# Kernel optimization log

Measured on AMD Instinct MI355X. Metric: run time of the kernel, lower is better.

## Reference

```python
import jax, jax.numpy as jnp
import numpy as np

D_MODEL = 1024
N_HEADS = 16
D_HEAD = D_MODEL // N_HEADS  # 64
D_VALUE = 64
D_FFN = 4096
B, T = 2, 2048
LN_EPS = 1e-5


def setup_inputs() -> dict:
    key = jax.random.key(0)
    ks = jax.random.split(key, 8)
    s = 0.02
    return {
        "x": jax.random.normal(ks[0], (B, T, D_MODEL), jnp.float32),
        "ln1_w": jnp.ones((D_MODEL,), jnp.float32),
        "ln1_b": jnp.zeros((D_MODEL,), jnp.float32),
        "Wq": jax.random.normal(ks[1], (D_MODEL, N_HEADS * D_HEAD), jnp.float32) * s,
        "Wk": jax.random.normal(ks[2], (D_MODEL, N_HEADS * D_HEAD), jnp.float32) * s,
        "Wv": jax.random.normal(ks[3], (D_MODEL, N_HEADS * D_VALUE), jnp.float32) * s,
        "Wo": jax.random.normal(ks[4], (N_HEADS * D_VALUE, D_MODEL), jnp.float32) * s,
        "ln2_w": jnp.ones((D_MODEL,), jnp.float32),
        "ln2_b": jnp.zeros((D_MODEL,), jnp.float32),
        "W1": jax.random.normal(ks[5], (D_MODEL, D_FFN), jnp.float32) * s,
        "W2": jax.random.normal(ks[6], (D_FFN, D_MODEL), jnp.float32) * s,
    }


def _layernorm(x, w, b):
    mu = jnp.mean(x, axis=-1, keepdims=True)
    var = jnp.mean(jnp.square(x - mu), axis=-1, keepdims=True)
    return (x - mu) * jax.lax.rsqrt(var + LN_EPS) * w + b


def reference(x, ln1_w, ln1_b, Wq, Wk, Wv, Wo, ln2_w, ln2_b, W1, W2):
    Bd, Td, Dd = x.shape
    h = _layernorm(x, ln1_w, ln1_b)
    # project and split heads: [B, H, T, d]
    Q = (h @ Wq).reshape(Bd, Td, N_HEADS, D_HEAD).transpose(0, 2, 1, 3)
    K = (h @ Wk).reshape(Bd, Td, N_HEADS, D_HEAD).transpose(0, 2, 1, 3)
    V = (h @ Wv).reshape(Bd, Td, N_HEADS, D_VALUE).transpose(0, 2, 1, 3)
    scale = 1.0 / np.sqrt(D_HEAD).astype(np.float32)
    scores = jnp.einsum("bhqd,bhkd->bhqk", Q, K) * scale  # [B,H,T,T]
    causal = jnp.tril(jnp.ones((Td, Td), bool))
    scores = jnp.where(causal[None, None], scores, -jnp.inf)
    attn = jax.nn.softmax(scores, axis=-1)
    out = jnp.einsum("bhqk,bhkd->bhqd", attn, V)  # [B,H,T,dv]
    out = out.transpose(0, 2, 1, 3).reshape(Bd, Td, N_HEADS * D_VALUE)
    x = x + out @ Wo
    h2 = _layernorm(x, ln2_w, ln2_b)
    # torch nn.GELU default is exact erf
    ffn = jax.nn.gelu(h2 @ W1, approximate=False) @ W2
    return x + ffn
```

## Files before the change

### kernel.cpp

```cpp
#include <hip/hip_runtime.h>

using short4_t = __attribute__((ext_vector_type(4))) short;
using short8_t = __attribute__((ext_vector_type(8))) short;
using f32x4    = __attribute__((ext_vector_type(4))) float;

#define B_SZ 2
#define T_SZ 2048
#define DM   1024
#define MROWS (B_SZ * T_SZ)

#define BAR() asm volatile("s_barrier" ::: "memory")

__device__ __forceinline__ unsigned short f2bf(float f) {
  unsigned u = __builtin_bit_cast(unsigned, f);
  return (unsigned short)((u + 0x7FFFu + ((u >> 16) & 1u)) >> 16);
}
__device__ __forceinline__ float bf2f(unsigned short u) {
  return __builtin_bit_cast(float, (unsigned)u << 16);
}

__device__ __forceinline__ f32x4 mfma32(short8_t a, short8_t b, f32x4 c) {
  return __builtin_amdgcn_mfma_f32_16x16x32_bf16(a, b, c, 0, 0, 0);
}
__device__ __forceinline__ f32x4 mfma16(short4_t a, short4_t b, f32x4 c) {
  return __builtin_amdgcn_mfma_f32_16x16x16bf16_1k(a, b, c, 0, 0, 0);
}

__device__ __forceinline__ void gload16(const void* g, void* l) {
  __builtin_amdgcn_global_load_lds(
      (const __attribute__((address_space(1))) unsigned int*)g,
      (__attribute__((address_space(3))) unsigned int*)l, 16, 0, 0);
}

__global__ __launch_bounds__(256) void transpose_all(
    const float* __restrict__ Wq, const float* __restrict__ Wk,
    const float* __restrict__ Wv, const float* __restrict__ Wo,
    const float* __restrict__ W1, const float* __restrict__ W2,
    unsigned short* __restrict__ WqkvT, unsigned short* __restrict__ WoT,
    unsigned short* __restrict__ W1T, unsigned short* __restrict__ W2T) {
  const int bid = blockIdx.x;
  const float* in;
  unsigned short* outp;
  int K, N, tn, tk;
  if (bid < 4096) {
    const int m = bid >> 10, t = bid & 1023;
    K = 1024; N = 1024; tn = t & 31; tk = t >> 5;
    in = (m == 0) ? Wq : (m == 1) ? Wk : (m == 2) ? Wv : Wo;
    outp = (m == 3) ? WoT : (WqkvT + (size_t)m * 1024 * 1024);
  } else if (bid < 8192) {
    const int t = bid - 4096;
    K = 1024; N = 4096; tn = t & 127; tk = t >> 7;
    in = W1; outp = W1T;
  } else {
    const int t = bid - 8192;
    K = 4096; N = 1024; tn = t & 31; tk = t >> 5;
    in = W2; outp = W2T;
  }
  __shared__ float tile[32][33];
  const int tx = threadIdx.x & 31, ty = threadIdx.x >> 5;
  const int n0 = tn * 32, k0 = tk * 32;
#pragma unroll
  for (int i = 0; i < 4; ++i)
    tile[ty + 8 * i][tx] = in[(size_t)(k0 + ty + 8 * i) * N + n0 + tx];
  __syncthreads();
#pragma unroll
  for (int i = 0; i < 4; ++i)
    outp[(size_t)(n0 + ty + 8 * i) * K + k0 + tx] = f2bf(tile[tx][ty + 8 * i]);
}

__global__ __launch_bounds__(256) void ln_kernel(
    const float* __restrict__ X, const float* __restrict__ W,
    const float* __restrict__ Bb, unsigned short* __restrict__ Out) {
  const int row = blockIdx.x, tid = threadIdx.x;
  const float4 v = *(const float4*)(X + (size_t)row * DM + tid * 4);
  float s1 = v.x + v.y + v.z + v.w;
  float s2 = v.x * v.x + v.y * v.y + v.z * v.z + v.w * v.w;
#pragma unroll
  for (int m = 1; m < 64; m <<= 1) {
    s1 += __shfl_xor(s1, m);
    s2 += __shfl_xor(s2, m);
  }
  __shared__ float red[8];
  const int wave = tid >> 6, lane = tid & 63;
  if (lane == 0) { red[wave * 2] = s1; red[wave * 2 + 1] = s2; }
  __syncthreads();
  const float S1 = red[0] + red[2] + red[4] + red[6];
  const float S2 = red[1] + red[3] + red[5] + red[7];
  const float mu = S1 * (1.0f / DM);
  const float var = S2 * (1.0f / DM) - mu * mu;
  const float rs = rsqrtf(var + 1e-5f);
  const float4 w = *(const float4*)(W + tid * 4);
  const float4 b = *(const float4*)(Bb + tid * 4);
  ushort4 o;
  o.x = f2bf((v.x - mu) * rs * w.x + b.x);
  o.y = f2bf((v.y - mu) * rs * w.y + b.y);
  o.z = f2bf((v.z - mu) * rs * w.z + b.z);
  o.w = f2bf((v.w - mu) * rs * w.w + b.w);
  *(ushort4*)(Out + (size_t)row * DM + tid * 4) = o;
}

template <int EPI>
__global__ __launch_bounds__(512, 2) void gemm8(
    const unsigned short* __restrict__ A, const unsigned short* __restrict__ Bt,
    const float* __restrict__ Res, void* __restrict__ Out,
    unsigned short* __restrict__ P01, unsigned short* __restrict__ P23,
    int N, int K, int Ksplit) {
  __shared__ char lds[3][32768];
  const int tid = threadIdx.x;
  const int lane = tid & 63;
  const int wave = tid >> 6;
  const int lr = lane & 15, lg = lane >> 4;
  const int wm = wave >> 2, wn = wave & 3;
  const int row0 = blockIdx.y * 256, col0 = blockIdx.x * 256;
  const int k0 = blockIdx.z * Ksplit;
  const int NT = Ksplit >> 5;

  size_t aoff[2], boff[2];
#pragma unroll
  for (int j = 0; j < 2; ++j) {
    const int o = j * 8192 + tid * 16;
    const int lrow = o >> 7, w = o & 127;
    const int u = w ^ ((lrow & 7) << 4);
    const int grow = lrow + ((u >> 6) << 7);
    const int gk = (u & 63) >> 1;
    aoff[j] = (size_t)(row0 + grow) * K + k0 + gk;
    boff[j] = (size_t)(col0 + grow) * K + k0 + gk;
  }
  const int axor = ((wm << 6) | (lg << 4)) ^ ((lr & 7) << 4);
  const int bxor = (((wn >> 1) << 6) | (lg << 4)) ^ ((lr & 7) << 4);
  const int arow = lr * 128;
  const int brow = ((wn & 1) * 64 + lr) * 128;

  f32x4 acc[8][4] = {};

#pragma unroll
  for (int t = 0; t < 2; ++t) {
#pragma unroll
    for (int j = 0; j < 2; ++j)
      gload16(A + aoff[j] + t * 32, &lds[t][0] + j * 8192 + tid * 16);
#pragma unroll
    for (int j = 0; j < 2; ++j)
      gload16(Bt + boff[j] + t * 32, &lds[t][0] + 16384 + j * 8192 + tid * 16);
  }
  asm volatile("s_waitcnt vmcnt(4)" ::: "memory");
  BAR();

  int bc = 0;
  for (int t = 0; t < NT; ++t) {
    const char* Acur = &lds[bc][0];
    const char* Bcur = Acur + 16384;
    int sb = bc + 2; if (sb >= 3) sb -= 3;
    char* Stg = &lds[sb][0];
    const int tko = (t + 2 < NT) ? (t + 2) * 32 : (NT - 1) * 32;

    short8_t af[4], bf[4];
#pragma unroll
    for (int rs = 0; rs < 4; ++rs)
      af[rs] = *(const short8_t*)(Acur + arow + rs * 2048 + axor);
#pragma unroll
    for (int cs = 0; cs < 4; ++cs)
      bf[cs] = *(const short8_t*)(Bcur + brow + cs * 2048 + bxor);
#pragma unroll
    for (int j = 0; j < 2; ++j)
      gload16(A + aoff[j] + tko, Stg + j * 8192 + tid * 16);
    BAR();
    __builtin_amdgcn_s_setprio(1);
#pragma unroll
    for (int rs = 0; rs < 4; ++rs)
#pragma unroll
      for (int cs = 0; cs < 4; ++cs)
        acc[rs][cs] = mfma32(af[rs], bf[cs], acc[rs][cs]);
    __builtin_amdgcn_s_setprio(0);
    BAR();

#pragma unroll
    for (int rs = 0; rs < 4; ++rs)
      af[rs] = *(const short8_t*)(Acur + arow + (rs + 4) * 2048 + axor);
#pragma unroll
    for (int j = 0; j < 2; ++j)
      gload16(Bt + boff[j] + tko, Stg + 16384 + j * 8192 + tid * 16);
    BAR();
    __builtin_amdgcn_s_setprio(1);
#pragma unroll
    for (int rs = 0; rs < 4; ++rs)
#pragma unroll
      for (int cs = 0; cs < 4; ++cs)
        acc[rs + 4][cs] = mfma32(af[rs], bf[cs], acc[rs + 4][cs]);
    __builtin_amdgcn_s_setprio(0);
    asm volatile("s_waitcnt vmcnt(4)" ::: "memory");
    BAR();
    bc = (bc == 2) ? 0 : bc + 1;
  }
  asm volatile("s_waitcnt vmcnt(0)" ::: "memory");

#pragma unroll
  for (int rs = 0; rs < 8; ++rs)
#pragma unroll
    for (int cs = 0; cs < 4; ++cs) {
      const int gr = row0 + wm * 128 + rs * 16 + lg * 4;
      const int gc = col0 + wn * 64 + cs * 16 + lr;
#pragma unroll
      for (int r = 0; r < 4; ++r) {
        const float v = acc[rs][cs][r];
        const size_t idx = (size_t)(gr + r) * N + gc;
        if (EPI == 0) {
          ((unsigned short*)Out)[idx] = f2bf(v);
        } else if (EPI == 1) {
          ((float*)Out)[idx] = v + Res[idx];
        } else if (EPI == 2) {
          const float g = 0.5f * v * (1.0f + erff(v * 0.70710678118654752f));
          ((unsigned short*)Out)[idx] = f2bf(g);
        } else {
          unsigned short* P = (blockIdx.z >> 1) ? P23 : P01;
          P[(size_t)(blockIdx.z & 1) * MROWS * 1024 + idx] = f2bf(v);
        }
      }
    }
}

__global__ __launch_bounds__(256) void reduce_ffn2(
    const float* __restrict__ X2,
    const unsigned short* __restrict__ P0, const unsigned short* __restrict__ P1,
    const unsigned short* __restrict__ P2, const unsigned short* __restrict__ P3,
    int ns, float* __restrict__ Out) {
  const size_t i = ((size_t)blockIdx.x * 256 + threadIdx.x) * 4;
  float4 o = *(const float4*)(X2 + i);
  ushort4 a = *(const ushort4*)(P0 + i);
  ushort4 b = *(const ushort4*)(P1 + i);
  o.x += bf2f(a.x) + bf2f(b.x);
  o.y += bf2f(a.y) + bf2f(b.y);
  o.z += bf2f(a.z) + bf2f(b.z);
  o.w += bf2f(a.w) + bf2f(b.w);
  if (ns == 4) {
    ushort4 c = *(const ushort4*)(P2 + i);
    ushort4 d = *(const ushort4*)(P3 + i);
    o.x += bf2f(c.x) + bf2f(d.x);
    o.y += bf2f(c.y) + bf2f(d.y);
    o.z += bf2f(c.z) + bf2f(d.z);
    o.w += bf2f(c.w) + bf2f(d.w);
  }
  *(float4*)(Out + i) = o;
}

__device__ __forceinline__ void attn_tile(
    const unsigned short* Kcur, const unsigned short* Vcur,
    const short8_t* qf, f32x4* acc, float& l_run, bool diag) {
  const int tid = threadIdx.x;
  const int lane = tid & 63, wave = tid >> 6;
  const int lr = lane & 15, lg = lane >> 4;
  const float C2 = 0.18033688011112042f;
  float pv[4][4];
  float psum = 0.f;
#pragma unroll
  for (int st = 0; st < 4; ++st) {
    f32x4 s = {0.f, 0.f, 0.f, 0.f};
#pragma unroll
    for (int c = 0; c < 2; ++c) {
      const int krow = st * 16 + lr;
      short8_t kf = *(const short8_t*)((const char*)Kcur + krow * 128 +
                                       ((c * 64 + lg * 16) ^ ((krow & 7) << 4)));
      s = mfma32(kf, qf[c], s);
    }
#pragma unroll
    for (int r = 0; r < 4; ++r) {
      float sv = s[r];
      if (diag) {
        const int keyl = st * 16 + lg * 4 + r;
        sv = (keyl <= wave * 16 + lr) ? sv : -3.0e38f;
      }
      const float p = exp2f(sv * C2);
      pv[st][r] = p;
      psum += p;
    }
  }
  psum += __shfl_xor(psum, 16);
  psum += __shfl_xor(psum, 32);
  l_run += psum;
  short4_t pa[4];
#pragma unroll
  for (int st = 0; st < 4; ++st) {
    unsigned u0, u1;
    asm("v_cvt_pk_bf16_f32 %0, %1, %2" : "=v"(u0) : "v"(pv[st][0]), "v"(pv[st][1]));
    asm("v_cvt_pk_bf16_f32 %0, %1, %2" : "=v"(u1) : "v"(pv[st][2]), "v"(pv[st][3]));
    uint2 uu;
    uu.x = u0; uu.y = u1;
    pa[st] = __builtin_bit_cast(short4_t, uu);
  }
#pragma unroll
  for (int st = 0; st < 4; ++st)
#pragma unroll
    for (int t = 0; t < 4; ++t) {
      const int row = t * 16 + lr;
      short4_t vb = *(const short4_t*)((const char*)Vcur + row * 128 +
                                       ((2 * (st * 16 + lg * 4)) ^ ((row & 7) << 4)));
      acc[t] = mfma16(pa[st], vb, acc[t]);
    }
}

__device__ __forceinline__ void attn_epilogue(
    const f32x4* acc, float l_run, int q0, int b, int h,
    unsigned short* __restrict__ out) {
  const int tid = threadIdx.x;
  const int lane = tid & 63, wave = tid >> 6;
  const int lr = lane & 15, lg = lane >> 4;
#pragma unroll
  for (int r = 0; r < 4; ++r) {
    const float lq = __shfl(l_run, lg * 4 + r);
    const float inv = 1.0f / lq;
    const int orow = q0 + wave * 16 + lg * 4 + r;
    const size_t obase = ((size_t)b * T_SZ + orow) * 1024 + h * 64 + lr;
#pragma unroll
    for (int t = 0; t < 4; ++t) out[obase + t * 16] = f2bf(acc[t][r] * inv);
  }
}

__global__ __launch_bounds__(256) void attn_kernel(
    const unsigned short* __restrict__ qkv, unsigned short* __restrict__ out) {
  __shared__ alignas(16) unsigned short Kl[2][64 * 64];
  __shared__ alignas(16) unsigned short Vt[2][64 * 64];
  const int tid = threadIdx.x;
  const int lane = tid & 63, wave = tid >> 6;
  const int lr = lane & 15, lg = lane >> 4;
  const int bid = blockIdx.x;
  const int pair = bid & 15, h = (bid >> 4) & 15, b = bid >> 8;
  const int qtA = pair, qtB = 31 - pair;
  const size_t rowbase = (size_t)b * T_SZ * 3072;
  const unsigned short* Qb = qkv + rowbase + h * 64;
  const unsigned short* Kb = qkv + rowbase + 1024 + h * 64;
  const unsigned short* Vb = qkv + rowbase + 2048 + h * 64;

  const int qrowA = qtA * 64 + wave * 16 + lr;
  const int qrowB = qtB * 64 + wave * 16 + lr;
  short8_t qfA[2], qfB[2];
#pragma unroll
  for (int c = 0; c < 2; ++c) {
    qfA[c] = *(const short8_t*)(Qb + (size_t)qrowA * 3072 + c * 32 + lg * 8);
    qfB[c] = *(const short8_t*)(Qb + (size_t)qrowB * 3072 + c * 32 + lg * 8);
  }
  f32x4 accA[4] = {}, accB[4] = {};
  float lA = 0.f, lB = 0.f;

  {
#pragma unroll
    for (int p = 0; p < 2; ++p) {
      const int o = p * 4096 + tid * 16;
      const int key = o >> 7, c0 = o & 127;
      const int csw = c0 ^ ((key & 7) << 4);
      gload16(Kb + (size_t)key * 3072 + (csw >> 1), (char*)Kl[0] + o);
    }
    const int vkey = tid & 63, wv = tid >> 6;
#pragma unroll
    for (int p = 0; p < 2; ++p) {
      const int dv0 = wv * 8 + p * 32;
      short8_t v = *(const short8_t*)(Vb + (size_t)vkey * 3072 + dv0);
#pragma unroll
      for (int e = 0; e < 8; ++e) {
        const int row = dv0 + e;
        *(unsigned short*)((char*)Vt[0] + row * 128 + ((2 * vkey) ^ ((row & 7) << 4))) =
            (unsigned short)v[e];
      }
    }
    __syncthreads();
  }

  int cur = 0;
  for (int i = 0; i <= qtB; ++i) {
    const int ktn = (i < qtB) ? i + 1 : qtB;
#pragma unroll
    for (int p = 0; p < 2; ++p) {
      const int o = p * 4096 + tid * 16;
      const int key = o >> 7, c0 = o & 127;
      const int csw = c0 ^ ((key & 7) << 4);
      gload16(Kb + (size_t)(ktn * 64 + key) * 3072 + (csw >> 1),
              (char*)Kl[cur ^ 1] + o);
    }
    const int vkey = lane;
    short8_t vr[2];
#pragma unroll
    for (int p = 0; p < 2; ++p) {
      const int dv0 = wave * 8 + p * 32;
      vr[p] = *(const short8_t*)(Vb + (size_t)(ktn * 64 + vkey) * 3072 + dv0);
    }

    if (i <= qtA)
      attn_tile(Kl[cur], Vt[cur], qfA, accA, lA, i == qtA);
    attn_tile(Kl[cur], Vt[cur], qfB, accB, lB, i == qtB);

#pragma unroll
    for (int p = 0; p < 2; ++p) {
      const int dv0 = wave * 8 + p * 32;
#pragma unroll
      for (int e = 0; e < 8; ++e) {
        const int row = dv0 + e;
        *(unsigned short*)((char*)Vt[cur ^ 1] + row * 128 +
                           ((2 * vkey) ^ ((row & 7) << 4))) = (unsigned short)vr[p][e];
      }
    }
    __syncthreads();
    cur ^= 1;
  }
  attn_epilogue(accA, lA, qtA * 64, b, h, out);
  attn_epilogue(accB, lB, qtB * 64, b, h, out);
}

extern "C" void kernel_launch(void* const* d_in, const int* in_sizes, int n_in,
                              void* d_out, int out_size, void* d_ws, size_t ws_size,
                              hipStream_t stream) {
  (void)in_sizes; (void)n_in; (void)out_size;
  const float* x    = (const float*)d_in[0];
  const float* ln1w = (const float*)d_in[1];
  const float* ln1b = (const float*)d_in[2];
  const float* Wq   = (const float*)d_in[3];
  const float* Wk   = (const float*)d_in[4];
  const float* Wv   = (const float*)d_in[5];
  const float* Wo   = (const float*)d_in[6];
  const float* ln2w = (const float*)d_in[7];
  const float* ln2b = (const float*)d_in[8];
  const float* W1   = (const float*)d_in[9];
  const float* W2   = (const float*)d_in[10];
  float* out = (float*)d_out;

  char* ws = (char*)d_ws;
  unsigned short* WqkvT = (unsigned short*)(ws + 0);
  unsigned short* WoT   = (unsigned short*)(ws + 6291456);
  unsigned short* W1T   = (unsigned short*)(ws + 8388608);
  unsigned short* W2T   = (unsigned short*)(ws + 16777216);
  unsigned short* H12   = (unsigned short*)(ws + 25165824);
  float*          X2    = (float*)(ws + 33554432);
  unsigned short* QKV   = (unsigned short*)(ws + 50331648);
  unsigned short* GBUF  = QKV;
  unsigned short* P0 = (unsigned short*)(ws + 0);
  unsigned short* P1 = (unsigned short*)(ws + 8388608);
  unsigned short* P2 = (unsigned short*)(ws + 83886080);
  unsigned short* P3 = (unsigned short*)(ws + 83886080 + 8388608);
  const bool big = ws_size >= 100663296ull;

  transpose_all<<<12288, 256, 0, stream>>>(Wq, Wk, Wv, Wo, W1, W2,
                                           WqkvT, WoT, W1T, W2T);
  ln_kernel<<<MROWS, 256, 0, stream>>>(x, ln1w, ln1b, H12);
  gemm8<0><<<dim3(12, 16, 1), 512, 0, stream>>>(H12, WqkvT, nullptr, QKV,
                                                nullptr, nullptr, 3072, 1024, 1024);
  attn_kernel<<<512, 256, 0, stream>>>(QKV, H12);
  gemm8<1><<<dim3(4, 16, 1), 512, 0, stream>>>(H12, WoT, x, X2,
                                               nullptr, nullptr, 1024, 1024, 1024);
  ln_kernel<<<MROWS, 256, 0, stream>>>(X2, ln2w, ln2b, H12);
  gemm8<2><<<dim3(16, 16, 1), 512, 0, stream>>>(H12, W1T, nullptr, GBUF,
                                                nullptr, nullptr, 4096, 1024, 1024);
  if (big) {
    gemm8<3><<<dim3(4, 16, 4), 512, 0, stream>>>(GBUF, W2T, nullptr, nullptr,
                                                 P0, P2, 1024, 4096, 1024);
    reduce_ffn2<<<4096, 256, 0, stream>>>(X2, P0, P1, P2, P3, 4, out);
  } else {
    gemm8<3><<<dim3(4, 16, 2), 512, 0, stream>>>(GBUF, W2T, nullptr, nullptr,
                                                 P0, nullptr, 1024, 4096, 2048);
    reduce_ffn2<<<4096, 256, 0, stream>>>(X2, P0, P1, nullptr, nullptr, 2, out);
  }
}
```

Before: 250.6 us.

## Split-K the output projection and fuse partial reduction with LayerNorm2

The Wo projection GEMM now runs split-K four ways, producing bf16 partials, so it launches 256 blocks instead of 64. A new reduce_ln kernel sums the partials with the residual, writes X2, and computes LayerNorm2 in the same pass, replacing the separate ln_kernel. The aim is better occupancy on the small GEMM and one fewer full pass over X2. In exchange, bf16 partials add rounding error, and the single-pass variance formula (E[x²]−mu²) is less numerically robust.

```diff
diff --git a/kernel.cpp b/kernel.cpp
--- a/kernel.cpp
+++ b/kernel.cpp
@@ -242,6 +242,49 @@
   *(float4*)(Out + i) = o;
 }
 
+__global__ __launch_bounds__(256) void reduce_ln(
+    const float* __restrict__ x,
+    const unsigned short* __restrict__ P01, const unsigned short* __restrict__ P23,
+    const float* __restrict__ W, const float* __restrict__ Bb,
+    float* __restrict__ X2, unsigned short* __restrict__ H12) {
+  const int row = blockIdx.x, tid = threadIdx.x;
+  const size_t base = (size_t)row * DM + tid * 4;
+  float4 v = *(const float4*)(x + base);
+  ushort4 a = *(const ushort4*)(P01 + base);
+  ushort4 b = *(const ushort4*)(P01 + (size_t)MROWS * DM + base);
+  ushort4 c = *(const ushort4*)(P23 + base);
+  ushort4 d = *(const ushort4*)(P23 + (size_t)MROWS * DM + base);
+  v.x += bf2f(a.x) + bf2f(b.x) + bf2f(c.x) + bf2f(d.x);
+  v.y += bf2f(a.y) + bf2f(b.y) + bf2f(c.y) + bf2f(d.y);
+  v.z += bf2f(a.z) + bf2f(b.z) + bf2f(c.z) + bf2f(d.z);
+  v.w += bf2f(a.w) + bf2f(b.w) + bf2f(c.w) + bf2f(d.w);
+  *(float4*)(X2 + base) = v;
+  float s1 = v.x + v.y + v.z + v.w;
+  float s2 = v.x * v.x + v.y * v.y + v.z * v.z + v.w * v.w;
+#pragma unroll
+  for (int m = 1; m < 64; m <<= 1) {
+    s1 += __shfl_xor(s1, m);
+    s2 += __shfl_xor(s2, m);
+  }
+  __shared__ float red[8];
+  const int wave = tid >> 6, lane = tid & 63;
+  if (lane == 0) { red[wave * 2] = s1; red[wave * 2 + 1] = s2; }
+  __syncthreads();
+  const float S1 = red[0] + red[2] + red[4] + red[6];
+  const float S2 = red[1] + red[3] + red[5] + red[7];
+  const float mu = S1 * (1.0f / DM);
+  const float var = S2 * (1.0f / DM) - mu * mu;
+  const float rs = rsqrtf(var + 1e-5f);
+  const float4 w = *(const float4*)(W + tid * 4);
+  const float4 bb = *(const float4*)(Bb + tid * 4);
+  ushort4 o;
+  o.x = f2bf((v.x - mu) * rs * w.x + bb.x);
+  o.y = f2bf((v.y - mu) * rs * w.y + bb.y);
+  o.z = f2bf((v.z - mu) * rs * w.z + bb.z);
+  o.w = f2bf((v.w - mu) * rs * w.w + bb.w);
+  *(ushort4*)(H12 + base) = o;
+}
+
 __device__ __forceinline__ void attn_tile(
     const unsigned short* Kcur, const unsigned short* Vcur,
     const short8_t* qf, f32x4* acc, float& l_run, bool diag) {
@@ -429,6 +472,8 @@
   float*          X2    = (float*)(ws + 33554432);
   unsigned short* QKV   = (unsigned short*)(ws + 50331648);
   unsigned short* GBUF  = QKV;
+  unsigned short* WoP01 = (unsigned short*)(ws + 50331648);
+  unsigned short* WoP23 = (unsigned short*)(ws + 67108864);
   unsigned short* P0 = (unsigned short*)(ws + 0);
   unsigned short* P1 = (unsigned short*)(ws + 8388608);
   unsigned short* P2 = (unsigned short*)(ws + 83886080);
@@ -441,9 +486,9 @@
   gemm8<0><<<dim3(12, 16, 1), 512, 0, stream>>>(H12, WqkvT, nullptr, QKV,
                                                 nullptr, nullptr, 3072, 1024, 1024);
   attn_kernel<<<512, 256, 0, stream>>>(QKV, H12);
-  gemm8<1><<<dim3(4, 16, 1), 512, 0, stream>>>(H12, WoT, x, X2,
-                                               nullptr, nullptr, 1024, 1024, 1024);
-  ln_kernel<<<MROWS, 256, 0, stream>>>(X2, ln2w, ln2b, H12);
+  gemm8<3><<<dim3(4, 16, 4), 512, 0, stream>>>(H12, WoT, nullptr, nullptr,
+                                               WoP01, WoP23, 1024, 1024, 256);
+  reduce_ln<<<MROWS, 256, 0, stream>>>(x, WoP01, WoP23, ln2w, ln2b, X2, H12);
   gemm8<2><<<dim3(16, 16, 1), 512, 0, stream>>>(H12, W1T, nullptr, GBUF,
                                                 nullptr, nullptr, 4096, 1024, 1024);
   if (big) {
```

New measurement: 239.2 us. 4.5% less time.
